# Kernel optimization log

Measured on AMD Instinct MI355X. Metric: run time of the kernel, lower is better.

The kernel has to match this reference:

```python
import jax, jax.numpy as jnp
import numpy as np

N_NODES = 50000
N_EDGES = 800000
D_IN, D_HID, D_OUT = 64, 64, 1


def gcn_layer(x, src, dst, W, b):
    """GCN conv: linear transform, then degree-normalized scatter-add over edges
    (with self-loops), matching x' = D^-1/2 (A+I) D^-1/2 X W^T + b."""
    n = x.shape[0]
    h = x @ W.T + b                                   # [N, out]
    deg = jax.ops.segment_sum(jnp.ones_like(dst, dtype=h.dtype), dst,
                              num_segments=n) + 1.0   # +1 for self-loop
    inv_sqrt_deg = jax.lax.rsqrt(deg)                 # [N]
    coef = inv_sqrt_deg[src] * inv_sqrt_deg[dst]      # [E]
    msgs = h[src] * coef[:, None]                     # gather + scale
    agg = jax.ops.segment_sum(msgs, dst, num_segments=n)   # scatter-add
    agg = agg + h * (inv_sqrt_deg * inv_sqrt_deg)[:, None]  # self-loop term
    return agg


def setup_inputs() -> dict:
    key = jax.random.key(0)
    k = jax.random.split(key, 9)
    x = jax.random.normal(k[0], (N_NODES, D_IN), dtype=jnp.float32)
    edge_index = jax.random.randint(k[1], (2, N_EDGES), 0, N_NODES, dtype=jnp.int64)
    s = 0.1
    W0 = jax.random.normal(k[2], (D_HID, D_IN), dtype=jnp.float32) * s
    b0 = jnp.zeros((D_HID,), dtype=jnp.float32)
    W1 = jax.random.normal(k[3], (D_HID, D_HID), dtype=jnp.float32) * s
    b1 = jnp.zeros((D_HID,), dtype=jnp.float32)
    W2 = jax.random.normal(k[4], (D_OUT, D_HID), dtype=jnp.float32) * s
    b2 = jnp.zeros((D_OUT,), dtype=jnp.float32)
    return {"x": x, "edge_index": edge_index,
            "W0": W0, "b0": b0, "W1": W1, "b1": b1, "W2": W2, "b2": b2}


def reference(x, edge_index, W0, b0, W1, b1, W2, b2):
    src, dst = edge_index[0], edge_index[1]
    h = jax.nn.relu(gcn_layer(x, src, dst, W0, b0))
    h = jax.nn.relu(gcn_layer(h, src, dst, W1, b1))
    out = gcn_layer(h, src, dst, W2, b2)   # [N, 1] per-node logits
    return out
```

## Files before the change

### kernel.cpp

```cpp
#include <hip/hip_runtime.h>

#define N_NODES 50000
#define N_EDGES 800000
#define DMAX 64
#define ZROW N_NODES
#define NB 196
#define CELL 40
#define P1_BLKS 512
#define LIN_BLKS 3125
typedef unsigned short u16;

__device__ __forceinline__ u16 f2bf(float f) {
    unsigned u = __builtin_bit_cast(unsigned, f);
    u += 0x7FFFu + ((u >> 16) & 1u);
    return (u16)(u >> 16);
}
__device__ __forceinline__ float bflo(unsigned u) {
    return __builtin_bit_cast(float, u << 16);
}
__device__ __forceinline__ float bfhi(unsigned u) {
    return __builtin_bit_cast(float, u & 0xFFFF0000u);
}

__global__ __launch_bounds__(256) void bin_lin0_k(
    const int* __restrict__ src, const int* __restrict__ dst,
    unsigned* __restrict__ payload, unsigned char* __restrict__ counts,
    const float* __restrict__ x, const float* __restrict__ W,
    const float* __restrict__ b, u16* __restrict__ hA)
{
    __shared__ float4 smem4[2009];
    int bid = blockIdx.x;
    int tid = threadIdx.x;
    if (bid < P1_BLKS) {
        unsigned* cur = (unsigned*)smem4;
        unsigned* pay = cur + NB;
        for (int i = tid; i < NB; i += 256) cur[i] = 0;
        __syncthreads();
        const int4* dst4 = (const int4*)dst;
        const int4* src4 = (const int4*)src;
        const int NQ = N_EDGES / 4;
        for (int q = bid * 256 + tid; q < NQ; q += P1_BLKS * 256) {
            int4 d = dst4[q];
            int4 s = src4[q];
#define BIN(dd, ss)                                                        \
            {                                                              \
                int bkt = (dd) >> 8;                                       \
                unsigned v = ((unsigned)(ss) << 8) | ((unsigned)(dd) & 255u); \
                int p = atomicAdd((int*)&cur[bkt], 1);                     \
                if (p < CELL) pay[bkt * CELL + p] = v;                     \
            }
            BIN(d.x, s.x) BIN(d.y, s.y) BIN(d.z, s.z) BIN(d.w, s.w)
#undef BIN
        }
        __syncthreads();
        unsigned* pg = payload + (size_t)bid * (NB * CELL);
        for (int i = tid; i < NB * CELL; i += 256) pg[i] = pay[i];
        for (int i = tid; i < NB; i += 256)
            counts[bid * NB + i] = (unsigned char)min((int)cur[i], CELL);
    } else {
        float* Ws = (float*)smem4;
        float* xs = (float*)smem4 + 64 * 68;
        int j = tid & 63, ln = tid >> 6;
        int nb = (bid - P1_BLKS) * 16;
        const float4* W4 = (const float4*)W;
#pragma unroll
        for (int i = 0; i < 4; ++i) {
            int idx4 = i * 256 + tid;
            *(float4*)&Ws[(idx4 >> 4) * 68 + (idx4 & 15) * 4] = W4[idx4];
        }
        {
            const float4* x4 = (const float4*)(x + (size_t)nb * 64);
            float4 v = x4[tid];
            *(float4*)&xs[(tid >> 4) * 68 + (tid & 15) * 4] = v;
        }
        __syncthreads();
        float a0 = b[j], a1 = a0, a2 = a0, a3 = a0;
        const float4* wp = (const float4*)&Ws[j * 68];
        const float4* p0 = (const float4*)&xs[(ln * 4 + 0) * 68];
        const float4* p1 = (const float4*)&xs[(ln * 4 + 1) * 68];
        const float4* p2 = (const float4*)&xs[(ln * 4 + 2) * 68];
        const float4* p3 = (const float4*)&xs[(ln * 4 + 3) * 68];
#pragma unroll
        for (int k4 = 0; k4 < 16; ++k4) {
            float4 w = wp[k4];
            float4 q0 = p0[k4]; a0 += w.x*q0.x + w.y*q0.y + w.z*q0.z + w.w*q0.w;
            float4 q1 = p1[k4]; a1 += w.x*q1.x + w.y*q1.y + w.z*q1.z + w.w*q1.w;
            float4 q2 = p2[k4]; a2 += w.x*q2.x + w.y*q2.y + w.z*q2.z + w.w*q2.w;
            float4 q3 = p3[k4]; a3 += w.x*q3.x + w.y*q3.y + w.z*q3.z + w.w*q3.w;
        }
        hA[(size_t)(nb + ln * 4 + 0) * 64 + j] = f2bf(a0);
        hA[(size_t)(nb + ln * 4 + 1) * 64 + j] = f2bf(a1);
        hA[(size_t)(nb + ln * 4 + 2) * 64 + j] = f2bf(a2);
        hA[(size_t)(nb + ln * 4 + 3) * 64 + j] = f2bf(a3);
    }
}

__global__ __launch_bounds__(256) void place_k(
    const unsigned* __restrict__ payload, const unsigned char* __restrict__ counts,
    int* __restrict__ cnt, u16* __restrict__ csr,
    u16* __restrict__ hA, u16* __restrict__ hB)
{
    __shared__ int cur[256];
    int b = blockIdx.x, tid = threadIdx.x;
    cur[tid] = 0;
    __syncthreads();
    int base = b << 8;
    for (int sb = tid; sb < P1_BLKS; sb += 256) {
        int c = counts[sb * NB + b];
        const unsigned* cell = payload + ((size_t)sb * NB + b) * CELL;
        for (int k = 0; k < c; ++k) {
            unsigned v = cell[k];
            int loc = (int)(v & 255u);
            int slot = atomicAdd(&cur[loc], 1);
            if (slot < DMAX) csr[(size_t)(base + loc) * 64 + slot] = (u16)(v >> 8);
        }
    }
    __syncthreads();
    int n = base + tid;
    if (n < N_NODES) {
        int c = cur[tid];
        cnt[n] = c;
        int m = min(c, DMAX);
        int mp = min((m + 15) & ~15, DMAX);
        for (int k = m; k < mp; ++k) csr[(size_t)n * 64 + k] = (u16)ZROW;
    }
    unsigned* hA32 = (unsigned*)hA;
    int col = tid & 31, r0 = tid >> 5;
    for (int it = 0; it < 32; ++it) {
        int rl = r0 + (it << 3);
        int n2 = base + rl;
        if (n2 < N_NODES) {
            float invn = rsqrtf((float)cur[rl] + 1.f);
            unsigned u = hA32[(size_t)n2 * 32 + col];
            float lo = bflo(u) * invn;
            float hi = bfhi(u) * invn;
            hA32[(size_t)n2 * 32 + col] = ((unsigned)f2bf(hi) << 16) | f2bf(lo);
        }
    }
    if (b == 0 && tid < 32) {
        ((unsigned*)hA)[(size_t)ZROW * 32 + tid] = 0;
        ((unsigned*)hB)[(size_t)ZROW * 32 + tid] = 0;
    }
}

#define PAIRB(k, AX, AY)                                                    \
    {                                                                       \
        int sa = __builtin_amdgcn_readlane(s_l, i + 2*(k));                 \
        int sb = __builtin_amdgcn_readlane(s_l, i + 2*(k) + 1);             \
        int ss = hsel ? sb : sa;                                            \
        unsigned uu = *(const unsigned*)(hb + (((size_t)ss) << 6) + fp);    \
        AX += bflo(uu); AY += bfhi(uu);                                     \
    }

#define GATHERB(hb, n, m16, TX, TY)                                         \
    int s_l = (int)csr[(size_t)(n) * 64 + j];                               \
    float ax0=0.f, ay0=0.f, ax1=0.f, ay1=0.f;                               \
    float ax2=0.f, ay2=0.f, ax3=0.f, ay3=0.f;                               \
    _Pragma("unroll 1")                                                     \
    for (int i = 0; i < (m16); i += 16) {                                   \
        PAIRB(0, ax0, ay0) PAIRB(1, ax1, ay1)                               \
        PAIRB(2, ax2, ay2) PAIRB(3, ax3, ay3)                               \
        PAIRB(4, ax0, ay0) PAIRB(5, ax1, ay1)                               \
        PAIRB(6, ax2, ay2) PAIRB(7, ax3, ay3)                               \
    }                                                                       \
    float TX = (ax0 + ax1) + (ax2 + ax3);                                   \
    float TY = (ay0 + ay1) + (ay2 + ay3);                                   \
    TX += __shfl_xor(TX, 32, 64);                                           \
    TY += __shfl_xor(TY, 32, 64);                                           \
    {                                                                       \
        unsigned su = *(const unsigned*)(hb + (((size_t)(n)) << 6) + fp);   \
        TX += bflo(su); TY += bfhi(su);                                     \
    }

__global__ __launch_bounds__(256) void gl_k(const u16* __restrict__ hb,
                                            const int* __restrict__ cnt,
                                            const u16* __restrict__ csr,
                                            const float* __restrict__ W,
                                            const float* __restrict__ b,
                                            u16* __restrict__ outb) {
    __shared__ float Ws[64 * 68];
    __shared__ float rs[4][68];
    int tid = threadIdx.x, j = tid & 63, w = tid >> 6;
    int fp = (j & 31) * 2, hsel = j >> 5;
    int nb = blockIdx.x * 16;
    const float4* W4 = (const float4*)W;
#pragma unroll
    for (int i = 0; i < 4; ++i) {
        int idx4 = i * 256 + tid;
        *(float4*)&Ws[(idx4 >> 4) * 68 + (idx4 & 15) * 4] = W4[idx4];
    }
    __syncthreads();
    const float4* wp = (const float4*)&Ws[j * 68];
    float bj = b[j];
#pragma unroll 1
    for (int t = 0; t < 4; ++t) {
        int n = nb + w * 4 + t;
        int mf = cnt[n];
        float invn = rsqrtf((float)mf + 1.f);
        int m16 = min((min(mf, DMAX) + 15) & ~15, DMAX);
        GATHERB(hb, n, m16, tx, ty)
        if (j < 32) {
            rs[w][fp]     = fmaxf(tx * invn, 0.f);
            rs[w][fp + 1] = fmaxf(ty * invn, 0.f);
        }
        __builtin_amdgcn_wave_barrier();
        float o0 = bj, o1 = 0.f;
        const float4* rp = (const float4*)&rs[w][0];
#pragma unroll
        for (int k4 = 0; k4 < 16; k4 += 2) {
            float4 w0 = wp[k4],     q0 = rp[k4];
            float4 w1 = wp[k4 + 1], q1 = rp[k4 + 1];
            o0 += w0.x*q0.x + w0.y*q0.y + w0.z*q0.z + w0.w*q0.w;
            o1 += w1.x*q1.x + w1.y*q1.y + w1.z*q1.z + w1.w*q1.w;
        }
        __builtin_amdgcn_wave_barrier();
        outb[(size_t)n * 64 + j] = f2bf((o0 + o1) * invn);
    }
}

__global__ __launch_bounds__(256) void gd_k(const u16* __restrict__ hb,
                                            const int* __restrict__ cnt,
                                            const u16* __restrict__ csr,
                                            const float* __restrict__ W2,
                                            const float* __restrict__ b2,
                                            float* __restrict__ h2) {
    int tid = threadIdx.x, j = tid & 63, w = tid >> 6;
    int fp = (j & 31) * 2, hsel = j >> 5;
    int nb = blockIdx.x * 16;
    float w2x = W2[fp], w2y = W2[fp + 1], b2s = b2[0];
#pragma unroll 1
    for (int t = 0; t < 4; ++t) {
        int n = nb + w * 4 + t;
        int mf = cnt[n];
        float invn = rsqrtf((float)mf + 1.f);
        int m16 = min((min(mf, DMAX) + 15) & ~15, DMAX);
        GATHERB(hb, n, m16, tx, ty)
        float c = fmaxf(tx * invn, 0.f) * w2x + fmaxf(ty * invn, 0.f) * w2y;
#pragma unroll
        for (int off = 16; off; off >>= 1) c += __shfl_xor(c, off, 64);
        if (j == 0) h2[n] = (c + b2s) * invn;
    }
}

__global__ __launch_bounds__(256) void g1_k(const float* __restrict__ h2,
                                            const int* __restrict__ cnt,
                                            const u16* __restrict__ csr,
                                            float* __restrict__ out) {
    int tid = threadIdx.x, j = tid & 63, w = tid >> 6;
    int nb = blockIdx.x * 16;
#pragma unroll 1
    for (int t = 0; t < 4; ++t) {
        int n = nb + w * 4 + t;
        int mf = cnt[n];
        int m = min(mf, DMAX);
        float invn = rsqrtf((float)mf + 1.f);
        float v = 0.f;
        if (j < m) v = h2[(int)csr[(size_t)n * 64 + j]];
#pragma unroll
        for (int off = 32; off; off >>= 1) v += __shfl_xor(v, off, 64);
        if (j == 0) out[n] = (v + h2[n]) * invn;
    }
}

extern "C" void kernel_launch(void* const* d_in, const int* in_sizes, int n_in,
                              void* d_out, int out_size, void* d_ws, size_t ws_size,
                              hipStream_t stream) {
    const float* x  = (const float*)d_in[0];
    const int*   ei = (const int*)d_in[1];
    const float* W0 = (const float*)d_in[2];
    const float* b0 = (const float*)d_in[3];
    const float* W1 = (const float*)d_in[4];
    const float* b1 = (const float*)d_in[5];
    const float* W2 = (const float*)d_in[6];
    const float* b2 = (const float*)d_in[7];
    float* out = (float*)d_out;

    char* ws = (char*)d_ws;
    size_t off = 0;
    auto alloc = [&](size_t bytes) {
        void* p = ws + off;
        off = (off + bytes + 255) & ~(size_t)255;
        return p;
    };
    int*      cnt  = (int*)alloc((size_t)N_NODES * 4);
    u16*      csr  = (u16*)alloc((size_t)N_NODES * DMAX * 2);
    u16*      hA   = (u16*)alloc((size_t)(N_NODES + 1) * 64 * 2);
    u16*      hB   = (u16*)alloc((size_t)(N_NODES + 1) * 64 * 2);
    float*    h2   = (float*)alloc((size_t)N_NODES * 4);
    unsigned* payload = (unsigned*)alloc((size_t)P1_BLKS * NB * CELL * 4);
    unsigned char* counts = (unsigned char*)alloc((size_t)P1_BLKS * NB);

    const int* src = ei;
    const int* dst = ei + N_EDGES;

    bin_lin0_k<<<P1_BLKS + LIN_BLKS, 256, 0, stream>>>(src, dst, payload, counts,
                                                       x, W0, b0, hA);
    place_k<<<NB, 256, 0, stream>>>(payload, counts, cnt, csr, hA, hB);
    gl_k<<<LIN_BLKS, 256, 0, stream>>>(hA, cnt, csr, W1, b1, hB);
    gd_k<<<LIN_BLKS, 256, 0, stream>>>(hB, cnt, csr, W2, b2, h2);
    g1_k<<<LIN_BLKS, 256, 0, stream>>>(h2, cnt, csr, out);
}
```

Before: 109.3 us.

## Switch hidden features to fp32 and gather four nodes per wave with float4 lanes

Stores the intermediate node features as fp32 instead of bf16 and rewrites the gather kernels so that each wave handles four nodes. Each 16-lane quarter loads float4 slices of a neighbour row, using CSR indices staged in shared memory instead of readlane broadcasts. W1 is held in registers, and the gather kernels launch fewer blocks that each cover 64 nodes. The aim is fewer, wider memory transactions and better lane use, but the fp32 rows double the bytes gathered per edge and the per-row padding in shared memory adds work.

New measurement: 126.6 us. 1.16x slower.

```diff
diff --git a/kernel.cpp b/kernel.cpp
--- a/kernel.cpp
+++ b/kernel.cpp
@@ -8,25 +8,14 @@
 #define CELL 40
 #define P1_BLKS 512
 #define LIN_BLKS 3125
+#define GBLK 782
 typedef unsigned short u16;
-
-__device__ __forceinline__ u16 f2bf(float f) {
-    unsigned u = __builtin_bit_cast(unsigned, f);
-    u += 0x7FFFu + ((u >> 16) & 1u);
-    return (u16)(u >> 16);
-}
-__device__ __forceinline__ float bflo(unsigned u) {
-    return __builtin_bit_cast(float, u << 16);
-}
-__device__ __forceinline__ float bfhi(unsigned u) {
-    return __builtin_bit_cast(float, u & 0xFFFF0000u);
-}
 
 __global__ __launch_bounds__(256) void bin_lin0_k(
     const int* __restrict__ src, const int* __restrict__ dst,
     unsigned* __restrict__ payload, unsigned char* __restrict__ counts,
     const float* __restrict__ x, const float* __restrict__ W,
-    const float* __restrict__ b, u16* __restrict__ hA)
+    const float* __restrict__ b, float* __restrict__ hA)
 {
     __shared__ float4 smem4[2009];
     int bid = blockIdx.x;
@@ -88,17 +77,17 @@
             float4 q2 = p2[k4]; a2 += w.x*q2.x + w.y*q2.y + w.z*q2.z + w.w*q2.w;
             float4 q3 = p3[k4]; a3 += w.x*q3.x + w.y*q3.y + w.z*q3.z + w.w*q3.w;
         }
-        hA[(size_t)(nb + ln * 4 + 0) * 64 + j] = f2bf(a0);
-        hA[(size_t)(nb + ln * 4 + 1) * 64 + j] = f2bf(a1);
-        hA[(size_t)(nb + ln * 4 + 2) * 64 + j] = f2bf(a2);
-        hA[(size_t)(nb + ln * 4 + 3) * 64 + j] = f2bf(a3);
+        hA[(size_t)(nb + ln * 4 + 0) * 64 + j] = a0;
+        hA[(size_t)(nb + ln * 4 + 1) * 64 + j] = a1;
+        hA[(size_t)(nb + ln * 4 + 2) * 64 + j] = a2;
+        hA[(size_t)(nb + ln * 4 + 3) * 64 + j] = a3;
     }
 }
 
 __global__ __launch_bounds__(256) void place_k(
     const unsigned* __restrict__ payload, const unsigned char* __restrict__ counts,
     int* __restrict__ cnt, u16* __restrict__ csr,
-    u16* __restrict__ hA, u16* __restrict__ hB)
+    float* __restrict__ hA, float* __restrict__ hB)
 {
     __shared__ int cur[256];
     int b = blockIdx.x, tid = threadIdx.x;
@@ -121,124 +110,135 @@
         int c = cur[tid];
         cnt[n] = c;
         int m = min(c, DMAX);
-        int mp = min((m + 15) & ~15, DMAX);
-        for (int k = m; k < mp; ++k) csr[(size_t)n * 64 + k] = (u16)ZROW;
-    }
-    unsigned* hA32 = (unsigned*)hA;
-    int col = tid & 31, r0 = tid >> 5;
-    for (int it = 0; it < 32; ++it) {
-        int rl = r0 + (it << 3);
-        int n2 = base + rl;
-        if (n2 < N_NODES) {
-            float invn = rsqrtf((float)cur[rl] + 1.f);
-            unsigned u = hA32[(size_t)n2 * 32 + col];
-            float lo = bflo(u) * invn;
-            float hi = bfhi(u) * invn;
-            hA32[(size_t)n2 * 32 + col] = ((unsigned)f2bf(hi) << 16) | f2bf(lo);
-        }
-    }
-    if (b == 0 && tid < 32) {
-        ((unsigned*)hA)[(size_t)ZROW * 32 + tid] = 0;
-        ((unsigned*)hB)[(size_t)ZROW * 32 + tid] = 0;
-    }
-}
-
-#define PAIRB(k, AX, AY)                                                    \
-    {                                                                       \
-        int sa = __builtin_amdgcn_readlane(s_l, i + 2*(k));                 \
-        int sb = __builtin_amdgcn_readlane(s_l, i + 2*(k) + 1);             \
-        int ss = hsel ? sb : sa;                                            \
-        unsigned uu = *(const unsigned*)(hb + (((size_t)ss) << 6) + fp);    \
-        AX += bflo(uu); AY += bfhi(uu);                                     \
-    }
-
-#define GATHERB(hb, n, m16, TX, TY)                                         \
-    int s_l = (int)csr[(size_t)(n) * 64 + j];                               \
-    float ax0=0.f, ay0=0.f, ax1=0.f, ay1=0.f;                               \
-    float ax2=0.f, ay2=0.f, ax3=0.f, ay3=0.f;                               \
-    _Pragma("unroll 1")                                                     \
-    for (int i = 0; i < (m16); i += 16) {                                   \
-        PAIRB(0, ax0, ay0) PAIRB(1, ax1, ay1)                               \
-        PAIRB(2, ax2, ay2) PAIRB(3, ax3, ay3)                               \
-        PAIRB(4, ax0, ay0) PAIRB(5, ax1, ay1)                               \
-        PAIRB(6, ax2, ay2) PAIRB(7, ax3, ay3)                               \
-    }                                                                       \
-    float TX = (ax0 + ax1) + (ax2 + ax3);                                   \
-    float TY = (ay0 + ay1) + (ay2 + ay3);                                   \
-    TX += __shfl_xor(TX, 32, 64);                                           \
-    TY += __shfl_xor(TY, 32, 64);                                           \
-    {                                                                       \
-        unsigned su = *(const unsigned*)(hb + (((size_t)(n)) << 6) + fp);   \
-        TX += bflo(su); TY += bfhi(su);                                     \
-    }
-
-__global__ __launch_bounds__(256) void gl_k(const u16* __restrict__ hb,
+        for (int k = m; k < DMAX; ++k) csr[(size_t)n * 64 + k] = (u16)ZROW;
+        float inv = rsqrtf((float)c + 1.f);
+        float4* row = (float4*)&hA[(size_t)n * 64];
+#pragma unroll
+        for (int i2 = 0; i2 < 16; ++i2) {
+            float4 t = row[i2];
+            t.x *= inv; t.y *= inv; t.z *= inv; t.w *= inv;
+            row[i2] = t;
+        }
+    }
+    if (b == 0 && tid < 64) {
+        hA[(size_t)ZROW * 64 + tid] = 0.f;
+        hB[(size_t)ZROW * 64 + tid] = 0.f;
+        csr[(size_t)ZROW * 64 + tid] = (u16)ZROW;
+        if (tid == 0) cnt[ZROW] = 0;
+    }
+}
+
+__device__ __forceinline__ float4 quad_gather(
+    const float* __restrict__ hT, const int* __restrict__ cnt,
+    const u16* __restrict__ csr, u16* cs_w ,
+    int nq, int j, int q, int r, float& invn_out, int& nmy_out)
+{
+#pragma unroll
+    for (int i = 0; i < 2; ++i) {
+        int u = i * 64 + j;
+        int row = u >> 5, c = u & 31;
+        int nn = nq + row;
+        nn = nn < N_NODES ? nn : ZROW;
+        *(unsigned*)&cs_w[row * 66 + c * 2] = ((const unsigned*)csr)[nn * 32 + c];
+    }
+    int nmy = nq + q;
+    nmy_out = nmy;
+    int nuse = nmy < N_NODES ? nmy : ZROW;
+    int mc = cnt[nuse];
+    float invn = rsqrtf((float)mc + 1.f);
+    invn_out = invn;
+    int m16 = min((min(mc, DMAX) + 15) & ~15, DMAX);
+    int kmax = m16;
+    kmax = max(kmax, __shfl_xor(kmax, 16, 64));
+    kmax = max(kmax, __shfl_xor(kmax, 32, 64));
+    __builtin_amdgcn_wave_barrier();
+    const float4* hT4 = (const float4*)hT;
+    float4 a = hT4[(unsigned)(nuse * 16 + r)];
+    float ax = a.x, ay = a.y, az = a.z, aw = a.w;
+    const u16* myrow = cs_w + q * 66;
+#pragma unroll 1
+    for (int k = 0; k < kmax; k += 8) {
+#pragma unroll
+        for (int u = 0; u < 8; ++u) {
+            int s = (int)myrow[k + u];
+            float4 v = hT4[(unsigned)((s << 4) | r)];
+            ax += v.x; ay += v.y; az += v.z; aw += v.w;
+        }
+    }
+    float4 outv; outv.x = ax; outv.y = ay; outv.z = az; outv.w = aw;
+    return outv;
+}
+
+__global__ __launch_bounds__(256) void gl_k(const float* __restrict__ hA,
                                             const int* __restrict__ cnt,
                                             const u16* __restrict__ csr,
                                             const float* __restrict__ W,
                                             const float* __restrict__ b,
-                                            u16* __restrict__ outb) {
-    __shared__ float Ws[64 * 68];
-    __shared__ float rs[4][68];
-    int tid = threadIdx.x, j = tid & 63, w = tid >> 6;
-    int fp = (j & 31) * 2, hsel = j >> 5;
-    int nb = blockIdx.x * 16;
+                                            float* __restrict__ out) {
+    __shared__ float rs[4][4][68];
+    __shared__ u16 cs[4][4][66];
+    int tid = threadIdx.x, j = tid & 63, w = tid >> 6, q = (tid >> 4) & 3, r = tid & 15;
+    float4 Wreg[16];
     const float4* W4 = (const float4*)W;
 #pragma unroll
-    for (int i = 0; i < 4; ++i) {
-        int idx4 = i * 256 + tid;
-        *(float4*)&Ws[(idx4 >> 4) * 68 + (idx4 & 15) * 4] = W4[idx4];
-    }
-    __syncthreads();
-    const float4* wp = (const float4*)&Ws[j * 68];
+    for (int i = 0; i < 16; ++i) Wreg[i] = W4[j * 16 + i];
     float bj = b[j];
 #pragma unroll 1
     for (int t = 0; t < 4; ++t) {
-        int n = nb + w * 4 + t;
-        int mf = cnt[n];
-        float invn = rsqrtf((float)mf + 1.f);
-        int m16 = min((min(mf, DMAX) + 15) & ~15, DMAX);
-        GATHERB(hb, n, m16, tx, ty)
-        if (j < 32) {
-            rs[w][fp]     = fmaxf(tx * invn, 0.f);
-            rs[w][fp + 1] = fmaxf(ty * invn, 0.f);
-        }
+        int nq = blockIdx.x * 64 + w * 16 + t * 4;
+        float invn; int nmy;
+        float4 acc = quad_gather(hA, cnt, csr, &cs[w][0][0], nq, j, q, r, invn, nmy);
+        float4 rr;
+        rr.x = fmaxf(acc.x * invn, 0.f);
+        rr.y = fmaxf(acc.y * invn, 0.f);
+        rr.z = fmaxf(acc.z * invn, 0.f);
+        rr.w = fmaxf(acc.w * invn, 0.f);
+        *(float4*)&rs[w][q][r * 4] = rr;
         __builtin_amdgcn_wave_barrier();
-        float o0 = bj, o1 = 0.f;
-        const float4* rp = (const float4*)&rs[w][0];
-#pragma unroll
-        for (int k4 = 0; k4 < 16; k4 += 2) {
-            float4 w0 = wp[k4],     q0 = rp[k4];
-            float4 w1 = wp[k4 + 1], q1 = rp[k4 + 1];
-            o0 += w0.x*q0.x + w0.y*q0.y + w0.z*q0.z + w0.w*q0.w;
-            o1 += w1.x*q1.x + w1.y*q1.y + w1.z*q1.z + w1.w*q1.w;
+#pragma unroll 1
+        for (int tt = 0; tt < 4; ++tt) {
+            float invs = __shfl(invn, tt * 16, 64);
+            const float4* rp = (const float4*)&rs[w][tt][0];
+            float o0 = bj, o1 = 0.f, o2 = 0.f, o3 = 0.f;
+#pragma unroll
+            for (int i = 0; i < 16; i += 4) {
+                float4 a0 = Wreg[i], a1 = Wreg[i+1], a2 = Wreg[i+2], a3 = Wreg[i+3];
+                float4 r0 = rp[i], r1 = rp[i+1], r2 = rp[i+2], r3 = rp[i+3];
+                o0 += a0.x*r0.x + a0.y*r0.y + a0.z*r0.z + a0.w*r0.w;
+                o1 += a1.x*r1.x + a1.y*r1.y + a1.z*r1.z + a1.w*r1.w;
+                o2 += a2.x*r2.x + a2.y*r2.y + a2.z*r2.z + a2.w*r2.w;
+                o3 += a3.x*r3.x + a3.y*r3.y + a3.z*r3.z + a3.w*r3.w;
+            }
+            int n2 = nq + tt;
+            if (n2 < N_NODES)
+                out[(size_t)n2 * 64 + j] = ((o0 + o1) + (o2 + o3)) * invs;
         }
         __builtin_amdgcn_wave_barrier();
-        outb[(size_t)n * 64 + j] = f2bf((o0 + o1) * invn);
-    }
-}
-
-__global__ __launch_bounds__(256) void gd_k(const u16* __restrict__ hb,
+    }
+}
+
+__global__ __launch_bounds__(256) void gd_k(const float* __restrict__ hB,
                                             const int* __restrict__ cnt,
                                             const u16* __restrict__ csr,
                                             const float* __restrict__ W2,
                                             const float* __restrict__ b2,
                                             float* __restrict__ h2) {
-    int tid = threadIdx.x, j = tid & 63, w = tid >> 6;
-    int fp = (j & 31) * 2, hsel = j >> 5;
-    int nb = blockIdx.x * 16;
-    float w2x = W2[fp], w2y = W2[fp + 1], b2s = b2[0];
+    __shared__ u16 cs[4][4][66];
+    int tid = threadIdx.x, j = tid & 63, w = tid >> 6, q = (tid >> 4) & 3, r = tid & 15;
+    float4 w24 = ((const float4*)W2)[r];
+    float b2s = b2[0];
 #pragma unroll 1
     for (int t = 0; t < 4; ++t) {
-        int n = nb + w * 4 + t;
-        int mf = cnt[n];
-        float invn = rsqrtf((float)mf + 1.f);
-        int m16 = min((min(mf, DMAX) + 15) & ~15, DMAX);
-        GATHERB(hb, n, m16, tx, ty)
-        float c = fmaxf(tx * invn, 0.f) * w2x + fmaxf(ty * invn, 0.f) * w2y;
-#pragma unroll
-        for (int off = 16; off; off >>= 1) c += __shfl_xor(c, off, 64);
-        if (j == 0) h2[n] = (c + b2s) * invn;
+        int nq = blockIdx.x * 64 + w * 16 + t * 4;
+        float invn; int nmy;
+        float4 acc = quad_gather(hB, cnt, csr, &cs[w][0][0], nq, j, q, r, invn, nmy);
+        float p = fmaxf(acc.x * invn, 0.f) * w24.x + fmaxf(acc.y * invn, 0.f) * w24.y
+                + fmaxf(acc.z * invn, 0.f) * w24.z + fmaxf(acc.w * invn, 0.f) * w24.w;
+        p += __shfl_xor(p, 1, 64);
+        p += __shfl_xor(p, 2, 64);
+        p += __shfl_xor(p, 4, 64);
+        p += __shfl_xor(p, 8, 64);
+        if (r == 0 && nmy < N_NODES) h2[nmy] = (p + b2s) * invn;
     }
 }
 
@@ -282,10 +282,10 @@
         off = (off + bytes + 255) & ~(size_t)255;
         return p;
     };
-    int*      cnt  = (int*)alloc((size_t)N_NODES * 4);
-    u16*      csr  = (u16*)alloc((size_t)N_NODES * DMAX * 2);
-    u16*      hA   = (u16*)alloc((size_t)(N_NODES + 1) * 64 * 2);
-    u16*      hB   = (u16*)alloc((size_t)(N_NODES + 1) * 64 * 2);
+    int*      cnt  = (int*)alloc((size_t)(N_NODES + 1) * 4);
+    u16*      csr  = (u16*)alloc((size_t)(N_NODES + 1) * DMAX * 2);
+    float*    hA   = (float*)alloc((size_t)(N_NODES + 1) * 64 * 4);
+    float*    hB   = (float*)alloc((size_t)(N_NODES + 1) * 64 * 4);
     float*    h2   = (float*)alloc((size_t)N_NODES * 4);
     unsigned* payload = (unsigned*)alloc((size_t)P1_BLKS * NB * CELL * 4);
     unsigned char* counts = (unsigned char*)alloc((size_t)P1_BLKS * NB);
@@ -296,7 +296,7 @@
     bin_lin0_k<<<P1_BLKS + LIN_BLKS, 256, 0, stream>>>(src, dst, payload, counts,
                                                        x, W0, b0, hA);
     place_k<<<NB, 256, 0, stream>>>(payload, counts, cnt, csr, hA, hB);
-    gl_k<<<LIN_BLKS, 256, 0, stream>>>(hA, cnt, csr, W1, b1, hB);
-    gd_k<<<LIN_BLKS, 256, 0, stream>>>(hB, cnt, csr, W2, b2, h2);
+    gl_k<<<GBLK, 256, 0, stream>>>(hA, cnt, csr, W1, b1, hB);
+    gd_k<<<GBLK, 256, 0, stream>>>(hB, cnt, csr, W2, b2, h2);
     g1_k<<<LIN_BLKS, 256, 0, stream>>>(h2, cnt, csr, out);
 }
```
